# Kernel optimization log

Measured on AMD Instinct MI355X. Metric: run time of the kernel, lower is better.

## Reference

```python
import jax, jax.numpy as jnp
from jax import lax
import numpy as np

# Config (matches init_kwargs)
V = 8           # num_variables
E = 256         # embed_dim
LAGS = 4
W = 64          # window_size
STEP = 16       # step_size
K = 512         # num_tokens (codebook size)
B = 32
S = 8256        # samples; (S - W) % STEP == 0 -> T = 512 windows
T = (S - W) // STEP
CONV_OUT = (W - LAGS) // LAGS + 1   # 16 positions after strided conv


def setup_inputs() -> dict:
    key = jax.random.key(0)
    ks = jax.random.split(key, 6)
    x = jax.random.normal(ks[0], (B, V, S), dtype=jnp.float32)
    conv_w = jax.random.normal(ks[1], (E, V, LAGS), dtype=jnp.float32) * 0.1
    conv_b = jax.random.normal(ks[2], (E,), dtype=jnp.float32) * 0.01
    lin_w = jax.random.normal(ks[3], (E, E * CONV_OUT), dtype=jnp.float32) * 0.02
    lin_b = jax.random.normal(ks[4], (E,), dtype=jnp.float32) * 0.01
    codebook = jax.random.normal(ks[5], (K, E), dtype=jnp.float32)
    return {"x": x, "conv_w": conv_w, "conv_b": conv_b,
            "lin_w": lin_w, "lin_b": lin_b, "codebook": codebook}


def _encode_windows(x, conv_w, conv_b, lin_w, lin_b):
    # Extract all sliding windows at once: starts [T], offsets [W] -> idx [T, W]
    starts = jnp.arange(T) * STEP
    idx = starts[:, None] + jnp.arange(W)[None, :]
    xw = x[:, :, idx]                         # [B, V, T, W]
    xw = xw.transpose(0, 2, 1, 3).reshape(B * T, V, W)  # batch all windows
    # TCN encoder: strided Conv1d(V->E, kernel=LAGS, stride=LAGS) + ReLU
    y = lax.conv_general_dilated(
        xw, conv_w, window_strides=(LAGS,), padding='VALID',
        dimension_numbers=('NCH', 'OIH', 'NCH'))   # [B*T, E, CONV_OUT]
    y = jax.nn.relu(y + conv_b[None, :, None])
    # Flatten + Linear -> embedding per window
    e = y.reshape(B * T, E * CONV_OUT) @ lin_w.T + lin_b  # [B*T, E]
    return e


def reference(x, conv_w, conv_b, lin_w, lin_b, codebook):
    e = _encode_windows(x, conv_w, conv_b, lin_w, lin_b)   # [B*T, E]
    # Vector quantization: nearest codebook entry by L2 distance
    d = (jnp.sum(e * e, axis=1, keepdims=True)
         - 2.0 * (e @ codebook.T)
         + jnp.sum(codebook * codebook, axis=1)[None, :])  # [B*T, K]
    idx = jnp.argmin(d, axis=1)                            # [B*T]
    q = codebook[idx]                                      # [B*T, E]
    # straight-through estimator (standard VQ forward value == q)
    out = e + lax.stop_gradient(q - e)
    return out.reshape(B, T, E)
```

## Files before the change

kernel.cpp:

```cpp
#include <hip/hip_runtime.h>

typedef _Float16 f16;
typedef _Float16 f16x4 __attribute__((ext_vector_type(4)));
typedef _Float16 f16x8 __attribute__((ext_vector_type(8)));
typedef float    f32x16 __attribute__((ext_vector_type(16)));

#define NB 32
#define TTOT 512
#define SSN 8256
#define PT 2064
#define EE 256
#define KCB 512

#define YB   ((size_t)NB*EE*PT*2)
#define LWB  ((size_t)EE*4096*2)
#define CBB  ((size_t)KCB*EE*2)
#define EBB  ((size_t)16384*EE*2)
#define OFF_Y0  ((size_t)0)
#define OFF_Y1  (YB)
#define OFF_LW0 (2*YB)
#define OFF_LW1 (2*YB + LWB)
#define OFF_CB0 (2*YB + 2*LWB)
#define OFF_CB1 (2*YB + 2*LWB + CBB)
#define OFF_HN  (2*YB + 2*LWB + 2*CBB)
#define OFF_E0  (OFF_HN + 4096)
#define OFF_E1  (OFF_E0 + EBB)
#define WS_NEED (OFF_E1 + EBB)

#define INV2048 4.8828125e-4f

struct h2 { f16 hi, lo; };
__device__ __forceinline__ h2 split2(float v) {
  h2 r;
  r.hi = (f16)v;
  r.lo = (f16)((v - (float)r.hi) * 2048.0f);
  return r;
}

__device__ __forceinline__ f16x8 ldsfrag(const f16* p) {
  union { f16x8 v8; f16x4 v4[2]; } u;
  u.v4[0] = *(const f16x4*)p;
  u.v4[1] = *(const f16x4*)(p + 4);
  return u.v8;
}

#define MFMA16(a,b,c) __builtin_amdgcn_mfma_f32_32x32x16_f16(a, b, c, 0, 0, 0)

__global__ __launch_bounds__(256, 2)
void k01(const float* __restrict__ lin_w, const float* __restrict__ cbk,
         f16* __restrict__ lwp0, f16* __restrict__ lwp1,
         f16* __restrict__ cbp0, f16* __restrict__ cbp1, float* __restrict__ hn,
         const float* __restrict__ x, const float* __restrict__ cw,
         const float* __restrict__ cb, f16* __restrict__ y0, f16* __restrict__ y1)
{
  __shared__ float part[4][32];
  const int tid = threadIdx.x;
  const int bix = blockIdx.x;
  if (bix < 272) {
    const int bid = bix;
    if (bid < 256) {
      const int eo = bid, nb = eo >> 5, lo = eo & 31;
      const int ep = tid;
      const float* src = lin_w + (size_t)eo * 4096 + ep * 16;
      float f[16];
      *(float4*)(f + 0)  = ((const float4*)src)[0];
      *(float4*)(f + 4)  = ((const float4*)src)[1];
      *(float4*)(f + 8)  = ((const float4*)src)[2];
      *(float4*)(f + 12) = ((const float4*)src)[3];
      union { f16x8 v; f16 e[8]; } a0, a1, b0, b1;
#pragma unroll
      for (int i = 0; i < 8; ++i) {
        { h2 s = split2(f[i]);     a0.e[i] = s.hi; a1.e[i] = s.lo; }
        { h2 s = split2(f[i + 8]); b0.e[i] = s.hi; b1.e[i] = s.lo; }
      }
      const size_t base = ((size_t)nb * 16384 + (size_t)ep * 64 + lo) * 8;
      *(f16x8*)(lwp0 + base)       = a0.v;
      *(f16x8*)(lwp0 + base + 256) = b0.v;
      *(f16x8*)(lwp1 + base)       = a1.v;
      *(f16x8*)(lwp1 + base + 256) = b1.v;
    } else {
      const int jb = bid - 256;
      const int lane = tid & 63, ksg = tid >> 6;
      const int hi = lane >> 5, lo = lane & 31;
      const int j = jb * 32 + lo;
      float s = 0.f;
#pragma unroll
      for (int kq = 0; kq < 4; ++kq) {
        const int ks = ksg * 4 + kq;
        const float* src = cbk + (size_t)j * 256 + ks * 16 + 8 * hi;
        float f[8];
        *(float4*)(f + 0) = ((const float4*)src)[0];
        *(float4*)(f + 4) = ((const float4*)src)[1];
        union { f16x8 v; f16 e[8]; } h0, h1;
#pragma unroll
        for (int i = 0; i < 8; ++i) {
          s = fmaf(f[i], f[i], s);
          h2 t = split2(f[i]); h0.e[i] = t.hi; h1.e[i] = t.lo;
        }
        const size_t base = ((size_t)jb * 1024 + (size_t)ks * 64 + lane) * 8;
        *(f16x8*)(cbp0 + base) = h0.v;
        *(f16x8*)(cbp1 + base) = h1.v;
      }
      s += __shfl_xor(s, 32, 64);
      if (lane < 32) part[ksg][lane] = s;
      __syncthreads();
      if (tid < 32)
        hn[jb * 32 + tid] = 0.5f * (part[0][tid] + part[1][tid] + part[2][tid] + part[3][tid]);
    }
  } else {
    const int bid = bix - 272;
    const int b = bid / 18, rem = bid % 18;
    const int eq = rem / 9, ptile = rem % 9;
    const int p = ptile * 256 + tid;
    const bool valid = p < PT;
    const int pc = valid ? p : (PT - 1);
    float4 xv[8];
#pragma unroll
    for (int v = 0; v < 8; ++v)
      xv[v] = *(const float4*)(x + ((size_t)b * 8 + v) * SSN + 4 * pc);
    const int e0 = eq * 128;
    float4 wc[8], wn[8];
#pragma unroll
    for (int v = 0; v < 8; ++v) wc[v] = *(const float4*)(cw + (size_t)e0 * 32 + v * 4);
    for (int ep = e0; ep < e0 + 128; ++ep) {
      const int epn = (ep + 1 < e0 + 128) ? ep + 1 : ep;
#pragma unroll
      for (int v = 0; v < 8; ++v) wn[v] = *(const float4*)(cw + (size_t)epn * 32 + v * 4);
      float a = cb[ep];
#pragma unroll
      for (int v = 0; v < 8; ++v) {
        a = fmaf(xv[v].x, wc[v].x, a);
        a = fmaf(xv[v].y, wc[v].y, a);
        a = fmaf(xv[v].z, wc[v].z, a);
        a = fmaf(xv[v].w, wc[v].w, a);
      }
      a = fmaxf(a, 0.f);
      if (valid) {
        const h2 s = split2(a);
        const size_t o = ((size_t)b * EE + ep) * PT + p;
        y0[o] = s.hi; y1[o] = s.lo;
      }
#pragma unroll
      for (int v = 0; v < 8; ++v) wc[v] = wn[v];
    }
  }
}

__global__ __launch_bounds__(512, 1)
void k2_linear(const f16* __restrict__ yh0, const f16* __restrict__ yh1,
               const f16* __restrict__ lwp0, const f16* __restrict__ lwp1,
               const float* __restrict__ lin_b,
               f16* __restrict__ eh0, f16* __restrict__ eh1)
{
  __shared__ __align__(16) f16 ysh[2][2][4][528];
  __shared__ __align__(16) f16 bsh[2][4][4][2][512];
  const int tid = threadIdx.x;
  const int sw = (blockIdx.x & 7) * 32 + (blockIdx.x >> 3);
  const int nh = sw >> 7, mt = sw & 127;
  const int b = mt >> 2;
  const int p0 = (mt & 3) * 512;
  const int lane = tid & 63, wv = tid >> 6;
  const int m = wv >> 1, nq = wv & 1;
  const int hi = lane >> 5, lo = lane & 31;
  const int aoff = 4 * (m * 32 + lo) + 8 * hi;

  const int bke = wv >> 1;
  const int bnb0 = (wv & 1) * 2;
  const f16* bs[2][2];
#pragma unroll
  for (int j = 0; j < 2; ++j) {
    bs[j][0] = lwp0 + ((size_t)(nh * 4 + bnb0 + j) * 256) * 512 + lane * 8;
    bs[j][1] = lwp1 + ((size_t)(nh * 4 + bnb0 + j) * 256) * 512 + lane * 8;
  }
  const int ylimb = wv >> 2, yke = wv & 3;
  const f16* ysrcp = ylimb ? yh1 : yh0;
  const size_t ybase0 = ((size_t)b * EE + yke) * PT + p0 + lane * 8;

  f32x16 accH[2], accL[2];
#pragma unroll
  for (int n = 0; n < 2; ++n)
#pragma unroll
    for (int r = 0; r < 16; ++r) { accH[n][r] = 0.f; accL[n][r] = 0.f; }

  {
    const size_t epo = (size_t)bke * 512;
    float4 br[4];
#pragma unroll
    for (int i = 0; i < 4; ++i) br[i] = *(const float4*)(bs[i >> 1][i & 1] + epo);
    const float4 ya = *(const float4*)(ysrcp + ybase0);
    float4 yb{};
    if (lane < 2) yb = *(const float4*)(ysrcp + ybase0 + 512);
#pragma unroll
    for (int i = 0; i < 4; ++i)
      *(float4*)&bsh[0][bke][bnb0 + (i >> 1)][i & 1][lane * 8] = br[i];
    f16* yd = &ysh[0][ylimb][yke][lane * 8];
    *(float4*)yd = ya;
    if (lane < 2) *(float4*)(yd + 512) = yb;
  }
  __syncthreads();

  for (int ss = 0; ss < 64; ++ss) {
    const int cur = ss & 1;
    const int ssn = (ss < 63) ? ss + 1 : 63;
    const size_t epo = (size_t)(ssn * 4 + bke) * 512;
    float4 br[4];
#pragma unroll
    for (int i = 0; i < 4; ++i) br[i] = *(const float4*)(bs[i >> 1][i & 1] + epo);
    const size_t yb0 = ybase0 + (size_t)ssn * 4 * PT;
    const float4 ya = *(const float4*)(ysrcp + yb0);
    float4 yb{};
    if (lane < 2) yb = *(const float4*)(ysrcp + yb0 + 512);

#pragma unroll
    for (int ke = 0; ke < 4; ++ke) {
      const f16x8 a0 = ldsfrag(&ysh[cur][0][ke][aoff]);
      const f16x8 a1 = ldsfrag(&ysh[cur][1][ke][aoff]);
#pragma unroll
      for (int n = 0; n < 2; ++n) {
        const f16x8 b0 = *(const f16x8*)&bsh[cur][ke][nq * 2 + n][0][lane * 8];
        const f16x8 b1 = *(const f16x8*)&bsh[cur][ke][nq * 2 + n][1][lane * 8];
        accH[n] = MFMA16(a0, b0, accH[n]);
        accL[n] = MFMA16(a0, b1, accL[n]);
        accL[n] = MFMA16(a1, b0, accL[n]);
      }
    }
    {
      const int nxt = cur ^ 1;
#pragma unroll
      for (int i = 0; i < 4; ++i)
        *(float4*)&bsh[nxt][bke][bnb0 + (i >> 1)][i & 1][lane * 8] = br[i];
      f16* yd = &ysh[nxt][ylimb][yke][lane * 8];
      *(float4*)yd = ya;
      if (lane < 2) *(float4*)(yd + 512) = yb;
    }
    __syncthreads();
  }

#pragma unroll
  for (int n = 0; n < 2; ++n) {
    const int eo = nh * 128 + (nq * 2 + n) * 32 + lo;
    const float lb = lin_b[eo];
#pragma unroll
    for (int r = 0; r < 16; ++r) {
      const int wloc = m * 32 + (r & 3) + 8 * (r >> 2) + 4 * hi;
      const float v = accH[n][r] + accL[n][r] * INV2048 + lb;
      const h2 s = split2(v);
      const size_t o = (size_t)(mt * 128 + wloc) * EE + eo;
      eh0[o] = s.hi; eh1[o] = s.lo;
    }
  }
}

__global__ __launch_bounds__(512, 1)
void k3_dist(const f16* __restrict__ eh0, const f16* __restrict__ eh1,
             const f16* __restrict__ cbp0, const f16* __restrict__ cbp1,
             const float* __restrict__ hn, const float* __restrict__ cbk,
             float* __restrict__ out)
{
  __shared__ __align__(16) f16 esh[2][64][136];
  __shared__ float scs[4][64];
  __shared__ int   scj[4][64];
  __shared__ int   bestj[64];
  const int tid = threadIdx.x;
  const int w0 = blockIdx.x * 64;
  const int lane = tid & 63, wv = tid >> 6;
  const int m = wv & 1, jg = wv >> 1;
  const int hi = lane >> 5, lo = lane & 31;

  const f16* pBp[4][2];
  float hnv[4];
#pragma unroll
  for (int q = 0; q < 4; ++q) {
    const int jb = jg * 4 + q;
    pBp[q][0] = cbp0 + ((size_t)jb * 1024 + lane) * 8;
    pBp[q][1] = cbp1 + ((size_t)jb * 1024 + lane) * 8;
    hnv[q] = hn[jb * 32 + lo];
  }
  f32x16 accH[4], accL[4];
#pragma unroll
  for (int q = 0; q < 4; ++q)
#pragma unroll
    for (int r = 0; r < 16; ++r) { accH[q][r] = 0.f; accL[q][r] = 0.f; }

  const int ar = m * 32 + lo;
  f16x8 BA[4][2], BB[4][2];
#pragma unroll
  for (int q = 0; q < 4; ++q) {
    BA[q][0] = *(const f16x8*)(pBp[q][0]);
    BA[q][1] = *(const f16x8*)(pBp[q][1]);
  }

  for (int kh = 0; kh < 2; ++kh) {
    if (kh) __syncthreads();
    {
      const int r = tid >> 3, c8 = tid & 7;
      const f16* s0 = eh0 + (size_t)(w0 + r) * EE + kh * 128;
      const f16* s1 = eh1 + (size_t)(w0 + r) * EE + kh * 128;
#pragma unroll
      for (int i = 0; i < 2; ++i) {
        const int c = (c8 * 2 + i) * 8;
        *(float4*)&esh[0][r][c] = *(const float4*)(s0 + c);
        *(float4*)&esh[1][r][c] = *(const float4*)(s1 + c);
      }
    }
    __syncthreads();
#pragma unroll
    for (int ksl = 0; ksl < 8; ++ksl) {
      const int ks = kh * 8 + ksl;
      const int ksn = (ks < 15) ? ks + 1 : 15;
      const f16x8 a0 = *(const f16x8*)(&esh[0][ar][0] + ksl * 16 + 8 * hi);
      const f16x8 a1 = *(const f16x8*)(&esh[1][ar][0] + ksl * 16 + 8 * hi);
      if ((ks & 1) == 0) {
#pragma unroll
        for (int q = 0; q < 4; ++q) {
          BB[q][0] = *(const f16x8*)(pBp[q][0] + (size_t)ksn * 512);
          BB[q][1] = *(const f16x8*)(pBp[q][1] + (size_t)ksn * 512);
        }
#pragma unroll
        for (int q = 0; q < 4; ++q) {
          accH[q] = MFMA16(a0, BA[q][0], accH[q]);
          accL[q] = MFMA16(a0, BA[q][1], accL[q]);
          accL[q] = MFMA16(a1, BA[q][0], accL[q]);
        }
      } else {
#pragma unroll
        for (int q = 0; q < 4; ++q) {
          BA[q][0] = *(const f16x8*)(pBp[q][0] + (size_t)ksn * 512);
          BA[q][1] = *(const f16x8*)(pBp[q][1] + (size_t)ksn * 512);
        }
#pragma unroll
        for (int q = 0; q < 4; ++q) {
          accH[q] = MFMA16(a0, BB[q][0], accH[q]);
          accL[q] = MFMA16(a0, BB[q][1], accL[q]);
          accL[q] = MFMA16(a1, BB[q][0], accL[q]);
        }
      }
    }
  }

#pragma unroll
  for (int r = 0; r < 16; ++r) {
    float bs = accH[0][r] + accL[0][r] * INV2048 - hnv[0];
    int   bj = (jg * 4 + 0) * 32 + lo;
#pragma unroll
    for (int q = 1; q < 4; ++q) {
      const float s = accH[q][r] + accL[q][r] * INV2048 - hnv[q];
      const int   j = (jg * 4 + q) * 32 + lo;
      if (s > bs) { bs = s; bj = j; }
    }
#pragma unroll
    for (int d = 1; d < 32; d <<= 1) {
      const float os = __shfl_xor(bs, d, 64);
      const int   oj = __shfl_xor(bj, d, 64);
      if (os > bs || (os == bs && oj < bj)) { bs = os; bj = oj; }
    }
    if (lo == 0) {
      const int wloc = m * 32 + (r & 3) + 8 * (r >> 2) + 4 * hi;
      scs[jg][wloc] = bs; scj[jg][wloc] = bj;
    }
  }
  __syncthreads();
  if (tid < 64) {
    float bs = scs[0][tid]; int bj = scj[0][tid];
#pragma unroll
    for (int g = 1; g < 4; ++g) {
      const float s = scs[g][tid]; const int j = scj[g][tid];
      if (s > bs || (s == bs && j < bj)) { bs = s; bj = j; }
    }
    bestj[tid] = bj;
  }
  __syncthreads();
  {
    const int rr = tid >> 6;
    const int c4 = (tid & 63) * 4;
#pragma unroll
    for (int pass = 0; pass < 8; ++pass) {
      const int r = pass * 8 + rr;
      const int jb = bestj[r];
      const float4 v = *(const float4*)(cbk + (size_t)jb * EE + c4);
      *(float4*)(out + (size_t)(w0 + r) * EE + c4) = v;
    }
  }
}

#define V 8
#define LAGS 4
#define WIN 64
#define STEP 16
#define CONV_OUT 16
#define WPB 16
#define TPB 256
#define NWORD 19
#define YSTRIDE 80
#define XSPAN 304
#define FOFF_YS   0
#define FOFF_XS   10240
#define FOFF_ES   10240
#define FOFF_SC   0
#define FOFF_SI   4096
#define FOFF_PS   8192
#define FOFF_PI   8448
#define FOFF_IW   8704
#define SMEM_FLOATS 14336

__device__ __forceinline__ float f4get(const float4& v, int i) {
  return i == 0 ? v.x : (i == 1 ? v.y : (i == 2 ? v.z : v.w));
}

__device__ __forceinline__ float conv_one(const float* xs, int p, const float4* cw, float cb0) {
  float a = cb0;
#pragma unroll
  for (int v = 0; v < V; ++v) {
    const float4 xv = *(const float4*)(xs + v * XSPAN + 4 * p);
    a = fmaf(xv.x, cw[v].x, a);
    a = fmaf(xv.y, cw[v].y, a);
    a = fmaf(xv.z, cw[v].z, a);
    a = fmaf(xv.w, cw[v].w, a);
  }
  return fmaxf(a, 0.0f);
}

__global__ __launch_bounds__(TPB, 2)
void tok_fused(const float* __restrict__ x, const float* __restrict__ conv_w,
               const float* __restrict__ conv_b, const float* __restrict__ lin_w,
               const float* __restrict__ lin_b, const float* __restrict__ cbk,
               float* __restrict__ out)
{
  __shared__ float smem[SMEM_FLOATS];
  float* ys = smem + FOFF_YS;
  float* xs = smem + FOFF_XS;
  float* es = smem + FOFF_ES;
  float* sc = smem + FOFF_SC;
  int*   si = (int*)(smem + FOFF_SI);
  float* ps = smem + FOFF_PS;
  int*   pi = (int*)(smem + FOFF_PI);
  int*   iw = (int*)(smem + FOFF_IW);
  const int tid = threadIdx.x;
  const int b   = blockIdx.x >> 5;
  const int t0  = (blockIdx.x & 31) * WPB;
  const float* xb = x + (size_t)b * V * SSN + (size_t)t0 * STEP;
#pragma unroll
  for (int v = 0; v < V; ++v)
    for (int j = tid; j < XSPAN; j += TPB)
      xs[v * XSPAN + j] = xb[(size_t)v * SSN + j];
  double accd[WPB];
#pragma unroll
  for (int w = 0; w < WPB; ++w) accd[w] = 0.0;
  for (int half = 0; half < 2; ++half) {
    __syncthreads();
    {
      const int ep  = half * 128 + (tid >> 1);
      const int row = ep & 127;
      float4 cw[V];
      const float4* cwp = (const float4*)(conv_w + (size_t)ep * (V * LAGS));
#pragma unroll
      for (int v = 0; v < V; ++v) cw[v] = cwp[v];
      const float cb0 = conv_b[ep];
      const int c0 = (tid & 1) ? 10 : 0;
      const int c1 = (tid & 1) ? NWORD : 10;
      for (int c = c0; c < c1; ++c) {
        const int p = 4 * c;
        float r0 = conv_one(xs, p + 0, cw, cb0);
        float r1 = conv_one(xs, p + 1, cw, cb0);
        float r2 = conv_one(xs, p + 2, cw, cb0);
        float r3 = conv_one(xs, p + 3, cw, cb0);
        *(float4*)(ys + row * YSTRIDE + 4 * c) = make_float4(r0, r1, r2, r3);
      }
    }
    __syncthreads();
    const float* lwbase = lin_w + (size_t)tid * (EE * CONV_OUT) + half * (128 * CONV_OUT);
    float4 nA, nB, nC, nD;
    {
      const float4* p4 = (const float4*)(lwbase);
      nA = p4[0]; nB = p4[1]; nC = p4[2]; nD = p4[3];
    }
    for (int er = 0; er < 128; ++er) {
      const float4 lA = nA, lB = nB, lC = nC, lD = nD;
      const int ern = (er + 1) & 127;
      {
        const float4* p4 = (const float4*)(lwbase + ern * CONV_OUT);
        nA = p4[0]; nB = p4[1]; nC = p4[2]; nD = p4[3];
      }
      float4 yr[NWORD];
      const float4* yp = (const float4*)(ys + er * YSTRIDE);
#pragma unroll
      for (int q = 0; q < NWORD; ++q) yr[q] = yp[q];
      float it[WPB];
#pragma unroll
      for (int w = 0; w < WPB; ++w) it[w] = 0.0f;
#pragma unroll
      for (int o = 0; o < CONV_OUT; ++o) {
        const float lw_o = f4get(o < 4 ? lA : (o < 8 ? lB : (o < 12 ? lC : lD)), o & 3);
#pragma unroll
        for (int w = 0; w < WPB; ++w) {
          const int p = 4 * w + o;
          it[w] = fmaf(lw_o, f4get(yr[p >> 2], p & 3), it[w]);
        }
      }
#pragma unroll
      for (int w = 0; w < WPB; ++w) accd[w] += (double)it[w];
    }
  }
#pragma unroll
  for (int w = 0; w < WPB; ++w)
    es[w * EE + tid] = (float)accd[w] + lin_b[tid];
  __syncthreads();
  float s_best[WPB];
  int   i_best[WPB];
#pragma unroll
  for (int jj = 0; jj < 2; ++jj) {
    const int j = tid + jj * 256;
    const float4* cbp = (const float4*)(cbk + (size_t)j * EE);
    double sdd[WPB];
    float  sd32[WPB];
#pragma unroll
    for (int w = 0; w < WPB; ++w) { sdd[w] = 0.0; sd32[w] = 0.f; }
    double ndd = 0.0;
    float  nd32 = 0.f;
    float4 c4n = cbp[0];
    for (int i16 = 0; i16 < 4; ++i16) {
      for (int i4i = 0; i4i < 16; ++i4i) {
        const int i4 = i16 * 16 + i4i;
        const float4 c4 = c4n;
        c4n = cbp[(i4 + 1 <= 63) ? (i4 + 1) : 63];
        nd32 = fmaf(c4.x, c4.x, nd32);
        nd32 = fmaf(c4.y, c4.y, nd32);
        nd32 = fmaf(c4.z, c4.z, nd32);
        nd32 = fmaf(c4.w, c4.w, nd32);
#pragma unroll
        for (int w = 0; w < WPB; ++w) {
          const float4 e4 = *(const float4*)(es + w * EE + i4 * 4);
          sd32[w] = fmaf(c4.x, e4.x, sd32[w]);
          sd32[w] = fmaf(c4.y, e4.y, sd32[w]);
          sd32[w] = fmaf(c4.z, e4.z, sd32[w]);
          sd32[w] = fmaf(c4.w, e4.w, sd32[w]);
        }
      }
#pragma unroll
      for (int w = 0; w < WPB; ++w) { sdd[w] += (double)sd32[w]; sd32[w] = 0.f; }
      ndd += (double)nd32; nd32 = 0.f;
    }
#pragma unroll
    for (int w = 0; w < WPB; ++w) {
      const float s = (float)(sdd[w] - 0.5 * ndd);
      if (jj == 0) { s_best[w] = s; i_best[w] = j; }
      else if (s > s_best[w]) { s_best[w] = s; i_best[w] = j; }
    }
  }
#pragma unroll
  for (int w = 0; w < WPB; ++w) {
    sc[w * EE + tid] = s_best[w];
    si[w * EE + tid] = i_best[w];
  }
  __syncthreads();
  {
    const int w = tid >> 4, seg = tid & 15;
    float mm = -INFINITY; int mi = 0x7fffffff;
    for (int t = seg * 16; t < seg * 16 + 16; ++t) {
      const float s = sc[w * EE + t];
      const int   jx = si[w * EE + t];
      if (s > mm || (s == mm && jx < mi)) { mm = s; mi = jx; }
    }
    ps[w * 16 + seg] = mm; pi[w * 16 + seg] = mi;
  }
  __syncthreads();
  if (tid < WPB) {
    const int w = tid;
    float mm = -INFINITY; int mi = 0x7fffffff;
    for (int t = 0; t < 16; ++t) {
      const float s = ps[w * 16 + t];
      const int   jx = pi[w * 16 + t];
      if (s > mm || (s == mm && jx < mi)) { mm = s; mi = jx; }
    }
    iw[w] = mi;
  }
  __syncthreads();
  const size_t outb = ((size_t)b * TTOT + t0) * EE;
#pragma unroll
  for (int w = 0; w < WPB; ++w)
    out[outb + (size_t)w * EE + tid] = cbk[(size_t)iw[w] * EE + tid];
}

extern "C" void kernel_launch(void* const* d_in, const int* in_sizes, int n_in,
                              void* d_out, int out_size, void* d_ws, size_t ws_size,
                              hipStream_t stream) {
  const float* x      = (const float*)d_in[0];
  const float* conv_w = (const float*)d_in[1];
  const float* conv_b = (const float*)d_in[2];
  const float* lin_w  = (const float*)d_in[3];
  const float* lin_b  = (const float*)d_in[4];
  const float* cbk    = (const float*)d_in[5];
  float* out = (float*)d_out;

  if (ws_size < WS_NEED) {
    tok_fused<<<dim3(32 * 32), dim3(TPB), 0, stream>>>(x, conv_w, conv_b, lin_w, lin_b, cbk, out);
    return;
  }
  char* ws = (char*)d_ws;
  f16*   y0   = (f16*)(ws + OFF_Y0);
  f16*   y1   = (f16*)(ws + OFF_Y1);
  f16*   lwp0 = (f16*)(ws + OFF_LW0);
  f16*   lwp1 = (f16*)(ws + OFF_LW1);
  f16*   cbp0 = (f16*)(ws + OFF_CB0);
  f16*   cbp1 = (f16*)(ws + OFF_CB1);
  float* hn   = (float*)(ws + OFF_HN);
  f16*   e0   = (f16*)(ws + OFF_E0);
  f16*   e1   = (f16*)(ws + OFF_E1);

  k01<<<848, 256, 0, stream>>>(lin_w, cbk, lwp0, lwp1, cbp0, cbp1, hn,
                               x, conv_w, conv_b, y0, y1);
  k2_linear<<<256, 512, 0, stream>>>(y0, y1, lwp0, lwp1, lin_b, e0, e1);
  k3_dist <<<256, 512, 0, stream>>>(e0, e1, cbp0, cbp1, hn, cbk, out);
}
```

Baseline: 185.3 us.

## Give each wave a 2x2 MFMA tile in k2_linear with 256 threads

The linear GEMM kernel drops from 512 to 256 threads per block. Each wave now computes a 2x2 grid of 32x32 output tiles, so every A and B fragment read from LDS feeds two MFMAs, halving LDS reads per MFMA. Global loads are issued two tiles ahead, with registers holding the next tile while the current one is computed. This doubles accumulator register use per thread and leaves fewer waves per CU to hide latency.

Result: slower. 308.0 us (+66.2%).

```diff
diff --git a/kernel.cpp b/kernel.cpp
--- a/kernel.cpp
+++ b/kernel.cpp
@@ -146,7 +146,7 @@
   }
 }
 
-__global__ __launch_bounds__(512, 1)
+__global__ __launch_bounds__(256, 1)
 void k2_linear(const f16* __restrict__ yh0, const f16* __restrict__ yh1,
                const f16* __restrict__ lwp0, const f16* __restrict__ lwp1,
                const float* __restrict__ lin_b,
@@ -160,95 +160,118 @@
   const int b = mt >> 2;
   const int p0 = (mt & 3) * 512;
   const int lane = tid & 63, wv = tid >> 6;
-  const int m = wv >> 1, nq = wv & 1;
+  const int mg = wv >> 1, ng = wv & 1;
   const int hi = lane >> 5, lo = lane & 31;
-  const int aoff = 4 * (m * 32 + lo) + 8 * hi;
-
-  const int bke = wv >> 1;
-  const int bnb0 = (wv & 1) * 2;
-  const f16* bs[2][2];
+  int aoffs[2];
+#pragma unroll
+  for (int m2 = 0; m2 < 2; ++m2)
+    aoffs[m2] = 4 * ((mg * 2 + m2) * 32 + lo) + 8 * hi;
+
+  const f16* pBsrc[8];
+#pragma unroll
+  for (int i = 0; i < 8; ++i) {
+    const int nb = i >> 1, limb = i & 1;
+    const f16* base = limb ? lwp1 : lwp0;
+    pBsrc[i] = base + ((size_t)(nh * 4 + nb) * 256 + wv) * 512 + lane * 8;
+  }
+  const f16* pYsrc[2];
 #pragma unroll
   for (int j = 0; j < 2; ++j) {
-    bs[j][0] = lwp0 + ((size_t)(nh * 4 + bnb0 + j) * 256) * 512 + lane * 8;
-    bs[j][1] = lwp1 + ((size_t)(nh * 4 + bnb0 + j) * 256) * 512 + lane * 8;
-  }
-  const int ylimb = wv >> 2, yke = wv & 3;
-  const f16* ysrcp = ylimb ? yh1 : yh0;
-  const size_t ybase0 = ((size_t)b * EE + yke) * PT + p0 + lane * 8;
-
-  f32x16 accH[2], accL[2];
-#pragma unroll
-  for (int n = 0; n < 2; ++n)
-#pragma unroll
-    for (int r = 0; r < 16; ++r) { accH[n][r] = 0.f; accL[n][r] = 0.f; }
-
-  {
-    const size_t epo = (size_t)bke * 512;
-    float4 br[4];
-#pragma unroll
-    for (int i = 0; i < 4; ++i) br[i] = *(const float4*)(bs[i >> 1][i & 1] + epo);
-    const float4 ya = *(const float4*)(ysrcp + ybase0);
-    float4 yb{};
-    if (lane < 2) yb = *(const float4*)(ysrcp + ybase0 + 512);
-#pragma unroll
-    for (int i = 0; i < 4; ++i)
-      *(float4*)&bsh[0][bke][bnb0 + (i >> 1)][i & 1][lane * 8] = br[i];
-    f16* yd = &ysh[0][ylimb][yke][lane * 8];
-    *(float4*)yd = ya;
-    if (lane < 2) *(float4*)(yd + 512) = yb;
-  }
+    const int r = wv * 2 + j, limb = r >> 2, ke = r & 3;
+    const f16* base = limb ? yh1 : yh0;
+    pYsrc[j] = base + ((size_t)b * EE + ke) * PT + p0 + lane * 8;
+  }
+  const int yrow[2] = { wv * 2, wv * 2 + 1 };
+
+  f32x16 accH[2][2], accL[2][2];
+#pragma unroll
+  for (int m2 = 0; m2 < 2; ++m2)
+#pragma unroll
+    for (int n2 = 0; n2 < 2; ++n2)
+#pragma unroll
+      for (int r = 0; r < 16; ++r) { accH[m2][n2][r] = 0.f; accL[m2][n2][r] = 0.f; }
+
+  float4 br[8], yr[2], ye[2];
+  const bool yext = lane < 2;
+
+#define LOAD_TILE(tt) do {                                                     \
+    const size_t bo = (size_t)(tt) * 2048;                                     \
+    _Pragma("unroll")                                                          \
+    for (int i = 0; i < 8; ++i) br[i] = *(const float4*)(pBsrc[i] + bo);       \
+    const size_t yo = (size_t)(tt) * 4 * PT;                                   \
+    _Pragma("unroll")                                                          \
+    for (int j = 0; j < 2; ++j) {                                              \
+      yr[j] = *(const float4*)(pYsrc[j] + yo);                                 \
+      if (yext) ye[j] = *(const float4*)(pYsrc[j] + yo + 512);                 \
+    }                                                                          \
+  } while (0)
+
+#define WRITE_TILE(bb) do {                                                    \
+    _Pragma("unroll")                                                          \
+    for (int i = 0; i < 8; ++i)                                                \
+      *(float4*)&bsh[bb][wv][i >> 1][i & 1][lane * 8] = br[i];                 \
+    _Pragma("unroll")                                                          \
+    for (int j = 0; j < 2; ++j) {                                              \
+      const int r = yrow[j];                                                   \
+      f16* yd = &ysh[bb][r >> 2][r & 3][lane * 8];                             \
+      *(float4*)yd = yr[j];                                                    \
+      if (yext) *(float4*)(yd + 512) = ye[j];                                  \
+    }                                                                          \
+  } while (0)
+
+  LOAD_TILE(0);
+  WRITE_TILE(0);
+  LOAD_TILE(1);
   __syncthreads();
 
   for (int ss = 0; ss < 64; ++ss) {
     const int cur = ss & 1;
-    const int ssn = (ss < 63) ? ss + 1 : 63;
-    const size_t epo = (size_t)(ssn * 4 + bke) * 512;
-    float4 br[4];
-#pragma unroll
-    for (int i = 0; i < 4; ++i) br[i] = *(const float4*)(bs[i >> 1][i & 1] + epo);
-    const size_t yb0 = ybase0 + (size_t)ssn * 4 * PT;
-    const float4 ya = *(const float4*)(ysrcp + yb0);
-    float4 yb{};
-    if (lane < 2) yb = *(const float4*)(ysrcp + yb0 + 512);
+    WRITE_TILE(cur ^ 1);
+    const int tl = (ss + 2 < 64) ? ss + 2 : 63;
+    LOAD_TILE(tl);
 
 #pragma unroll
     for (int ke = 0; ke < 4; ++ke) {
-      const f16x8 a0 = ldsfrag(&ysh[cur][0][ke][aoff]);
-      const f16x8 a1 = ldsfrag(&ysh[cur][1][ke][aoff]);
-#pragma unroll
-      for (int n = 0; n < 2; ++n) {
-        const f16x8 b0 = *(const f16x8*)&bsh[cur][ke][nq * 2 + n][0][lane * 8];
-        const f16x8 b1 = *(const f16x8*)&bsh[cur][ke][nq * 2 + n][1][lane * 8];
-        accH[n] = MFMA16(a0, b0, accH[n]);
-        accL[n] = MFMA16(a0, b1, accL[n]);
-        accL[n] = MFMA16(a1, b0, accL[n]);
-      }
-    }
-    {
-      const int nxt = cur ^ 1;
-#pragma unroll
-      for (int i = 0; i < 4; ++i)
-        *(float4*)&bsh[nxt][bke][bnb0 + (i >> 1)][i & 1][lane * 8] = br[i];
-      f16* yd = &ysh[nxt][ylimb][yke][lane * 8];
-      *(float4*)yd = ya;
-      if (lane < 2) *(float4*)(yd + 512) = yb;
+      f16x8 a[2][2], bb[2][2];
+#pragma unroll
+      for (int m2 = 0; m2 < 2; ++m2) {
+        a[m2][0] = ldsfrag(&ysh[cur][0][ke][aoffs[m2]]);
+        a[m2][1] = ldsfrag(&ysh[cur][1][ke][aoffs[m2]]);
+      }
+#pragma unroll
+      for (int n2 = 0; n2 < 2; ++n2) {
+        bb[n2][0] = *(const f16x8*)&bsh[cur][ke][ng * 2 + n2][0][lane * 8];
+        bb[n2][1] = *(const f16x8*)&bsh[cur][ke][ng * 2 + n2][1][lane * 8];
+      }
+#pragma unroll
+      for (int m2 = 0; m2 < 2; ++m2)
+#pragma unroll
+        for (int n2 = 0; n2 < 2; ++n2) {
+          accH[m2][n2] = MFMA16(a[m2][0], bb[n2][0], accH[m2][n2]);
+          accL[m2][n2] = MFMA16(a[m2][0], bb[n2][1], accL[m2][n2]);
+          accL[m2][n2] = MFMA16(a[m2][1], bb[n2][0], accL[m2][n2]);
+        }
     }
     __syncthreads();
   }
 
 #pragma unroll
-  for (int n = 0; n < 2; ++n) {
-    const int eo = nh * 128 + (nq * 2 + n) * 32 + lo;
-    const float lb = lin_b[eo];
-#pragma unroll
-    for (int r = 0; r < 16; ++r) {
-      const int wloc = m * 32 + (r & 3) + 8 * (r >> 2) + 4 * hi;
-      const float v = accH[n][r] + accL[n][r] * INV2048 + lb;
-      const h2 s = split2(v);
-      const size_t o = (size_t)(mt * 128 + wloc) * EE + eo;
-      eh0[o] = s.hi; eh1[o] = s.lo;
-    }
-  }
+  for (int m2 = 0; m2 < 2; ++m2)
+#pragma unroll
+    for (int n2 = 0; n2 < 2; ++n2) {
+      const int eo = nh * 128 + (ng * 2 + n2) * 32 + lo;
+      const float lb = lin_b[eo];
+#pragma unroll
+      for (int r = 0; r < 16; ++r) {
+        const int wloc = (mg * 2 + m2) * 32 + (r & 3) + 8 * (r >> 2) + 4 * hi;
+        const float v = accH[m2][n2][r] + accL[m2][n2][r] * INV2048 + lb;
+        const h2 s = split2(v);
+        const size_t o = (size_t)(mt * 128 + wloc) * EE + eo;
+        eh0[o] = s.hi; eh1[o] = s.lo;
+      }
+    }
+#undef LOAD_TILE
+#undef WRITE_TILE
 }
 
 __global__ __launch_bounds__(512, 1)
@@ -609,6 +632,6 @@
 
   k01<<<848, 256, 0, stream>>>(lin_w, cbk, lwp0, lwp1, cbp0, cbp1, hn,
                                x, conv_w, conv_b, y0, y1);
-  k2_linear<<<256, 512, 0, stream>>>(y0, y1, lwp0, lwp1, lin_b, e0, e1);
+  k2_linear<<<256, 256, 0, stream>>>(y0, y1, lwp0, lwp1, lin_b, e0, e1);
   k3_dist <<<256, 512, 0, stream>>>(e0, e1, cbp0, cbp1, hn, cbk, out);
 }
```

## Split linear GEMM over K into two halves with atomic fp32 accumulation

Applied to the files above, without the earlier changes.

The linear layer kernel now splits the reduction dimension in two, launching twice as many blocks that each accumulate partial results into an fp32 buffer with atomicAdd. LDS double buffering is dropped to allow more resident blocks. Bias addition and the hi/lo fp16 split move into the distance kernel's load stage. This targets low occupancy on a 256-block launch, at the cost of a memset, fp32 atomics, extra global traffic and an extra barrier per step.

Result: slower. 272.4 us (+47.0%).

```diff
diff --git a/kernel.cpp b/kernel.cpp
--- a/kernel.cpp
+++ b/kernel.cpp
@@ -26,6 +26,7 @@
 #define OFF_E0  (OFF_HN + 4096)
 #define OFF_E1  (OFF_E0 + EBB)
 #define WS_NEED (OFF_E1 + EBB)
+#define PACC_BYTES ((size_t)16384*EE*4)
 
 #define INV2048 4.8828125e-4f
 
@@ -146,35 +147,31 @@
   }
 }
 
-__global__ __launch_bounds__(512, 1)
-void k2_linear(const f16* __restrict__ yh0, const f16* __restrict__ yh1,
-               const f16* __restrict__ lwp0, const f16* __restrict__ lwp1,
-               const float* __restrict__ lin_b,
-               f16* __restrict__ eh0, f16* __restrict__ eh1)
+__global__ __launch_bounds__(512, 4)
+void k2p(const f16* __restrict__ yh0, const f16* __restrict__ yh1,
+         const f16* __restrict__ lwp0, const f16* __restrict__ lwp1,
+         float* __restrict__ pacc)
 {
-  __shared__ __align__(16) f16 ysh[2][2][4][528];
-  __shared__ __align__(16) f16 bsh[2][4][4][2][512];
+  __shared__ __align__(16) f16 ysh[2][4][528];
+  __shared__ __align__(16) f16 bsh[4][4][2][512];
   const int tid = threadIdx.x;
-  const int sw = (blockIdx.x & 7) * 32 + (blockIdx.x >> 3);
-  const int nh = sw >> 7, mt = sw & 127;
-  const int b = mt >> 2;
+  const int sw = (blockIdx.x & 7) * 64 + (blockIdx.x >> 3);
+  const int kh = sw >> 8;
+  const int rest = sw & 255;
+  const int mt = rest >> 1, nh = rest & 1;
+  const int b  = mt >> 2;
   const int p0 = (mt & 3) * 512;
   const int lane = tid & 63, wv = tid >> 6;
-  const int m = wv >> 1, nq = wv & 1;
+  const int mg = wv >> 1, nqw = wv & 1;
   const int hi = lane >> 5, lo = lane & 31;
-  const int aoff = 4 * (m * 32 + lo) + 8 * hi;
-
-  const int bke = wv >> 1;
-  const int bnb0 = (wv & 1) * 2;
-  const f16* bs[2][2];
-#pragma unroll
-  for (int j = 0; j < 2; ++j) {
-    bs[j][0] = lwp0 + ((size_t)(nh * 4 + bnb0 + j) * 256) * 512 + lane * 8;
-    bs[j][1] = lwp1 + ((size_t)(nh * 4 + bnb0 + j) * 256) * 512 + lane * 8;
-  }
+
+  const int bke = wv >> 1, bnb0 = (wv & 1) * 2;
+  const f16* bs00 = lwp0 + ((size_t)(nh * 4 + bnb0) * 256 + kh * 128 + bke) * 512 + lane * 8;
+  const f16* bs01 = lwp1 + ((size_t)(nh * 4 + bnb0) * 256 + kh * 128 + bke) * 512 + lane * 8;
   const int ylimb = wv >> 2, yke = wv & 3;
   const f16* ysrcp = ylimb ? yh1 : yh0;
-  const size_t ybase0 = ((size_t)b * EE + yke) * PT + p0 + lane * 8;
+  const size_t ybase0 = ((size_t)b * EE + kh * 128 + yke) * PT + p0 + lane * 8;
+  const bool yext = lane < 2;
 
   f32x16 accH[2], accL[2];
 #pragma unroll
@@ -182,77 +179,71 @@
 #pragma unroll
     for (int r = 0; r < 16; ++r) { accH[n][r] = 0.f; accL[n][r] = 0.f; }
 
-  {
-    const size_t epo = (size_t)bke * 512;
-    float4 br[4];
-#pragma unroll
-    for (int i = 0; i < 4; ++i) br[i] = *(const float4*)(bs[i >> 1][i & 1] + epo);
-    const float4 ya = *(const float4*)(ysrcp + ybase0);
-    float4 yb{};
-    if (lane < 2) yb = *(const float4*)(ysrcp + ybase0 + 512);
-#pragma unroll
-    for (int i = 0; i < 4; ++i)
-      *(float4*)&bsh[0][bke][bnb0 + (i >> 1)][i & 1][lane * 8] = br[i];
-    f16* yd = &ysh[0][ylimb][yke][lane * 8];
-    *(float4*)yd = ya;
-    if (lane < 2) *(float4*)(yd + 512) = yb;
-  }
+  float4 br[4], ya; float4 yb{};
+
+#define K2LOAD(ss_) do {                                                       \
+    const size_t bo = (size_t)(ss_) * 2048;                                    \
+    br[0] = *(const float4*)(bs00 + bo);                                       \
+    br[1] = *(const float4*)(bs01 + bo);                                       \
+    br[2] = *(const float4*)(bs00 + 131072 + bo);                              \
+    br[3] = *(const float4*)(bs01 + 131072 + bo);                              \
+    const size_t yo = ybase0 + (size_t)(ss_) * (4 * PT);                       \
+    ya = *(const float4*)(ysrcp + yo);                                         \
+    if (yext) yb = *(const float4*)(ysrcp + yo + 512);                         \
+  } while (0)
+
+#define K2WRITE() do {                                                         \
+    *(float4*)&bsh[bke][bnb0    ][0][lane * 8] = br[0];                        \
+    *(float4*)&bsh[bke][bnb0    ][1][lane * 8] = br[1];                        \
+    *(float4*)&bsh[bke][bnb0 + 1][0][lane * 8] = br[2];                        \
+    *(float4*)&bsh[bke][bnb0 + 1][1][lane * 8] = br[3];                        \
+    f16* yd = &ysh[ylimb][yke][lane * 8];                                      \
+    *(float4*)yd = ya;                                                         \
+    if (yext) *(float4*)(yd + 512) = yb;                                       \
+  } while (0)
+
+  K2LOAD(0);
+  K2WRITE();
   __syncthreads();
 
-  for (int ss = 0; ss < 64; ++ss) {
-    const int cur = ss & 1;
-    const int ssn = (ss < 63) ? ss + 1 : 63;
-    const size_t epo = (size_t)(ssn * 4 + bke) * 512;
-    float4 br[4];
-#pragma unroll
-    for (int i = 0; i < 4; ++i) br[i] = *(const float4*)(bs[i >> 1][i & 1] + epo);
-    const size_t yb0 = ybase0 + (size_t)ssn * 4 * PT;
-    const float4 ya = *(const float4*)(ysrcp + yb0);
-    float4 yb{};
-    if (lane < 2) yb = *(const float4*)(ysrcp + yb0 + 512);
-
+  for (int ss = 0; ss < 32; ++ss) {
+    K2LOAD((ss < 31) ? ss + 1 : 31);
+
+    const int aoff = 4 * (mg * 32 + lo) + 8 * hi;
 #pragma unroll
     for (int ke = 0; ke < 4; ++ke) {
-      const f16x8 a0 = ldsfrag(&ysh[cur][0][ke][aoff]);
-      const f16x8 a1 = ldsfrag(&ysh[cur][1][ke][aoff]);
+      const f16x8 a0 = ldsfrag(&ysh[0][ke][aoff]);
+      const f16x8 a1 = ldsfrag(&ysh[1][ke][aoff]);
 #pragma unroll
       for (int n = 0; n < 2; ++n) {
-        const f16x8 b0 = *(const f16x8*)&bsh[cur][ke][nq * 2 + n][0][lane * 8];
-        const f16x8 b1 = *(const f16x8*)&bsh[cur][ke][nq * 2 + n][1][lane * 8];
+        const f16x8 b0 = *(const f16x8*)&bsh[ke][nqw * 2 + n][0][lane * 8];
+        const f16x8 b1 = *(const f16x8*)&bsh[ke][nqw * 2 + n][1][lane * 8];
         accH[n] = MFMA16(a0, b0, accH[n]);
         accL[n] = MFMA16(a0, b1, accL[n]);
         accL[n] = MFMA16(a1, b0, accL[n]);
       }
     }
-    {
-      const int nxt = cur ^ 1;
-#pragma unroll
-      for (int i = 0; i < 4; ++i)
-        *(float4*)&bsh[nxt][bke][bnb0 + (i >> 1)][i & 1][lane * 8] = br[i];
-      f16* yd = &ysh[nxt][ylimb][yke][lane * 8];
-      *(float4*)yd = ya;
-      if (lane < 2) *(float4*)(yd + 512) = yb;
-    }
     __syncthreads();
-  }
+    K2WRITE();
+    __syncthreads();
+  }
+#undef K2LOAD
+#undef K2WRITE
 
 #pragma unroll
   for (int n = 0; n < 2; ++n) {
-    const int eo = nh * 128 + (nq * 2 + n) * 32 + lo;
-    const float lb = lin_b[eo];
+    const int eo = nh * 128 + (nqw * 2 + n) * 32 + lo;
 #pragma unroll
     for (int r = 0; r < 16; ++r) {
-      const int wloc = m * 32 + (r & 3) + 8 * (r >> 2) + 4 * hi;
-      const float v = accH[n][r] + accL[n][r] * INV2048 + lb;
-      const h2 s = split2(v);
-      const size_t o = (size_t)(mt * 128 + wloc) * EE + eo;
-      eh0[o] = s.hi; eh1[o] = s.lo;
+      const int wloc = mg * 32 + (r & 3) + 8 * (r >> 2) + 4 * hi;
+      const float v = accH[n][r] + accL[n][r] * INV2048;
+      atomicAdd(&pacc[(size_t)(mt * 128 + wloc) * EE + eo], v);
     }
   }
 }
 
 __global__ __launch_bounds__(512, 1)
-void k3_dist(const f16* __restrict__ eh0, const f16* __restrict__ eh1,
+void k3_dist(const float* __restrict__ pacc, const float* __restrict__ lin_b,
              const f16* __restrict__ cbp0, const f16* __restrict__ cbp1,
              const float* __restrict__ hn, const float* __restrict__ cbk,
              float* __restrict__ out)
@@ -294,14 +285,25 @@
     if (kh) __syncthreads();
     {
       const int r = tid >> 3, c8 = tid & 7;
-      const f16* s0 = eh0 + (size_t)(w0 + r) * EE + kh * 128;
-      const f16* s1 = eh1 + (size_t)(w0 + r) * EE + kh * 128;
-#pragma unroll
-      for (int i = 0; i < 2; ++i) {
-        const int c = (c8 * 2 + i) * 8;
-        *(float4*)&esh[0][r][c] = *(const float4*)(s0 + c);
-        *(float4*)&esh[1][r][c] = *(const float4*)(s1 + c);
-      }
+      const float* ps = pacc + (size_t)(w0 + r) * EE + kh * 128 + c8 * 16;
+      const float* bsp = lin_b + kh * 128 + c8 * 16;
+      float f[16], bb[16];
+#pragma unroll
+      for (int i = 0; i < 4; ++i) {
+        *(float4*)(f + 4 * i)  = ((const float4*)ps)[i];
+        *(float4*)(bb + 4 * i) = ((const float4*)bsp)[i];
+      }
+      union { f16x8 v; f16 e[8]; } h0[2], h1[2];
+#pragma unroll
+      for (int i = 0; i < 16; ++i) {
+        const h2 s = split2(f[i] + bb[i]);
+        h0[i >> 3].e[i & 7] = s.hi;
+        h1[i >> 3].e[i & 7] = s.lo;
+      }
+      *(f16x8*)&esh[0][r][c8 * 16]     = h0[0].v;
+      *(f16x8*)&esh[0][r][c8 * 16 + 8] = h0[1].v;
+      *(f16x8*)&esh[1][r][c8 * 16]     = h1[0].v;
+      *(f16x8*)&esh[1][r][c8 * 16 + 8] = h1[1].v;
     }
     __syncthreads();
 #pragma unroll
@@ -604,11 +606,11 @@
   f16*   cbp0 = (f16*)(ws + OFF_CB0);
   f16*   cbp1 = (f16*)(ws + OFF_CB1);
   float* hn   = (float*)(ws + OFF_HN);
-  f16*   e0   = (f16*)(ws + OFF_E0);
-  f16*   e1   = (f16*)(ws + OFF_E1);
-
+  float* pacc = (float*)(ws + OFF_E0);
+
+  hipMemsetAsync(pacc, 0, PACC_BYTES, stream);
   k01<<<848, 256, 0, stream>>>(lin_w, cbk, lwp0, lwp1, cbp0, cbp1, hn,
                                x, conv_w, conv_b, y0, y1);
-  k2_linear<<<256, 512, 0, stream>>>(y0, y1, lwp0, lwp1, lin_b, e0, e1);
-  k3_dist <<<256, 512, 0, stream>>>(e0, e1, cbp0, cbp1, hn, cbk, out);
-}
+  k2p<<<512, 512, 0, stream>>>(y0, y1, lwp0, lwp1, pacc);
+  k3_dist<<<256, 512, 0, stream>>>(pacc, lin_b, cbp0, cbp1, hn, cbk, out);
+}
```

## Split linear GEMM along K into two partial-sum halves, reduce in distance kernel

Applied to the files above, without the earlier changes.

The linear layer GEMM is split into two K halves, giving 512 blocks instead of 256 and more parallelism across CUs. Each half writes fp32 partial sums to a new workspace region. The distance kernel adds the halves plus bias and splits the result into hi/lo fp16 before the codebook MFMA. This costs extra fp32 traffic for the partial buffers and needs a larger workspace, with a fallback to the old path when the workspace is too small.

New measurement: 252.6 us. 36.3% more time.

```diff
diff --git a/kernel.cpp b/kernel.cpp
--- a/kernel.cpp
+++ b/kernel.cpp
@@ -26,6 +26,9 @@
 #define OFF_E0  (OFF_HN + 4096)
 #define OFF_E1  (OFF_E0 + EBB)
 #define WS_NEED (OFF_E1 + EBB)
+#define PACC_BYTES ((size_t)16384*EE*4)
+#define OFF_P1  (WS_NEED)
+#define WS_NEED2 (WS_NEED + PACC_BYTES)
 
 #define INV2048 4.8828125e-4f
 
@@ -146,6 +149,252 @@
   }
 }
 
+__global__ __launch_bounds__(512, 4)
+void k2p(const f16* __restrict__ yh0, const f16* __restrict__ yh1,
+         const f16* __restrict__ lwp0, const f16* __restrict__ lwp1,
+         float* __restrict__ pacc0, float* __restrict__ pacc1)
+{
+  __shared__ __align__(16) f16 ysh[2][4][528];
+  __shared__ __align__(16) f16 bsh[4][4][2][512];
+  const int tid = threadIdx.x;
+  const int sw = (blockIdx.x & 7) * 64 + (blockIdx.x >> 3);
+  const int kh = sw >> 8;
+  const int rest = sw & 255;
+  const int mt = rest >> 1, nh = rest & 1;
+  const int b  = mt >> 2;
+  const int p0 = (mt & 3) * 512;
+  const int lane = tid & 63, wv = tid >> 6;
+  const int mg = wv >> 1, nqw = wv & 1;
+  const int hi = lane >> 5, lo = lane & 31;
+
+  const int bke = wv >> 1, bnb0 = (wv & 1) * 2;
+  const f16* bs00 = lwp0 + ((size_t)(nh * 4 + bnb0) * 256 + kh * 128 + bke) * 512 + lane * 8;
+  const f16* bs01 = lwp1 + ((size_t)(nh * 4 + bnb0) * 256 + kh * 128 + bke) * 512 + lane * 8;
+  const int ylimb = wv >> 2, yke = wv & 3;
+  const f16* ysrcp = ylimb ? yh1 : yh0;
+  const size_t ybase0 = ((size_t)b * EE + kh * 128 + yke) * PT + p0 + lane * 8;
+  const bool yext = lane < 2;
+
+  f32x16 accH[2], accL[2];
+#pragma unroll
+  for (int n = 0; n < 2; ++n)
+#pragma unroll
+    for (int r = 0; r < 16; ++r) { accH[n][r] = 0.f; accL[n][r] = 0.f; }
+
+  float4 br[4], ya; float4 yb{};
+
+#define K2LOAD(ss_) do {                                                       \
+    const size_t bo = (size_t)(ss_) * 2048;                                    \
+    br[0] = *(const float4*)(bs00 + bo);                                       \
+    br[1] = *(const float4*)(bs01 + bo);                                       \
+    br[2] = *(const float4*)(bs00 + 131072 + bo);                              \
+    br[3] = *(const float4*)(bs01 + 131072 + bo);                              \
+    const size_t yo = ybase0 + (size_t)(ss_) * (4 * PT);                       \
+    ya = *(const float4*)(ysrcp + yo);                                         \
+    if (yext) yb = *(const float4*)(ysrcp + yo + 512);                         \
+  } while (0)
+
+#define K2WRITE() do {                                                         \
+    *(float4*)&bsh[bke][bnb0    ][0][lane * 8] = br[0];                        \
+    *(float4*)&bsh[bke][bnb0    ][1][lane * 8] = br[1];                        \
+    *(float4*)&bsh[bke][bnb0 + 1][0][lane * 8] = br[2];                        \
+    *(float4*)&bsh[bke][bnb0 + 1][1][lane * 8] = br[3];                        \
+    f16* yd = &ysh[ylimb][yke][lane * 8];                                      \
+    *(float4*)yd = ya;                                                         \
+    if (yext) *(float4*)(yd + 512) = yb;                                       \
+  } while (0)
+
+  K2LOAD(0);
+  K2WRITE();
+  __syncthreads();
+
+  for (int ss = 0; ss < 32; ++ss) {
+    K2LOAD((ss < 31) ? ss + 1 : 31);
+
+    const int aoff = 4 * (mg * 32 + lo) + 8 * hi;
+#pragma unroll
+    for (int ke = 0; ke < 4; ++ke) {
+      const f16x8 a0 = ldsfrag(&ysh[0][ke][aoff]);
+      const f16x8 a1 = ldsfrag(&ysh[1][ke][aoff]);
+#pragma unroll
+      for (int n = 0; n < 2; ++n) {
+        const f16x8 b0 = *(const f16x8*)&bsh[ke][nqw * 2 + n][0][lane * 8];
+        const f16x8 b1 = *(const f16x8*)&bsh[ke][nqw * 2 + n][1][lane * 8];
+        accH[n] = MFMA16(a0, b0, accH[n]);
+        accL[n] = MFMA16(a0, b1, accL[n]);
+        accL[n] = MFMA16(a1, b0, accL[n]);
+      }
+    }
+    __syncthreads();
+    K2WRITE();
+    __syncthreads();
+  }
+#undef K2LOAD
+#undef K2WRITE
+
+  float* pacc = kh ? pacc1 : pacc0;
+#pragma unroll
+  for (int n = 0; n < 2; ++n) {
+    const int eo = nh * 128 + (nqw * 2 + n) * 32 + lo;
+#pragma unroll
+    for (int r = 0; r < 16; ++r) {
+      const int wloc = mg * 32 + (r & 3) + 8 * (r >> 2) + 4 * hi;
+      pacc[(size_t)(mt * 128 + wloc) * EE + eo] = accH[n][r] + accL[n][r] * INV2048;
+    }
+  }
+}
+
+__global__ __launch_bounds__(512, 1)
+void k3s(const float* __restrict__ pacc0, const float* __restrict__ pacc1,
+         const float* __restrict__ lin_b,
+         const f16* __restrict__ cbp0, const f16* __restrict__ cbp1,
+         const float* __restrict__ hn, const float* __restrict__ cbk,
+         float* __restrict__ out)
+{
+  __shared__ __align__(16) f16 esh[2][64][136];
+  __shared__ float scs[4][64];
+  __shared__ int   scj[4][64];
+  __shared__ int   bestj[64];
+  const int tid = threadIdx.x;
+  const int w0 = blockIdx.x * 64;
+  const int lane = tid & 63, wv = tid >> 6;
+  const int m = wv & 1, jg = wv >> 1;
+  const int hi = lane >> 5, lo = lane & 31;
+
+  const f16* pBp[4][2];
+  float hnv[4];
+#pragma unroll
+  for (int q = 0; q < 4; ++q) {
+    const int jb = jg * 4 + q;
+    pBp[q][0] = cbp0 + ((size_t)jb * 1024 + lane) * 8;
+    pBp[q][1] = cbp1 + ((size_t)jb * 1024 + lane) * 8;
+    hnv[q] = hn[jb * 32 + lo];
+  }
+  f32x16 accH[4], accL[4];
+#pragma unroll
+  for (int q = 0; q < 4; ++q)
+#pragma unroll
+    for (int r = 0; r < 16; ++r) { accH[q][r] = 0.f; accL[q][r] = 0.f; }
+
+  const int ar = m * 32 + lo;
+  f16x8 BA[4][2], BB[4][2];
+#pragma unroll
+  for (int q = 0; q < 4; ++q) {
+    BA[q][0] = *(const f16x8*)(pBp[q][0]);
+    BA[q][1] = *(const f16x8*)(pBp[q][1]);
+  }
+
+  for (int kh = 0; kh < 2; ++kh) {
+    if (kh) __syncthreads();
+    {
+      const int r = tid >> 3, c8 = tid & 7;
+      const size_t idx = (size_t)(w0 + r) * EE + kh * 128 + c8 * 16;
+      const float* ps0 = pacc0 + idx;
+      const float* ps1 = pacc1 + idx;
+      const float* bsp = lin_b + kh * 128 + c8 * 16;
+      float f[16];
+#pragma unroll
+      for (int i = 0; i < 4; ++i) {
+        const float4 v0 = ((const float4*)ps0)[i];
+        const float4 v1 = ((const float4*)ps1)[i];
+        const float4 bb = ((const float4*)bsp)[i];
+        f[4 * i + 0] = v0.x + v1.x + bb.x;
+        f[4 * i + 1] = v0.y + v1.y + bb.y;
+        f[4 * i + 2] = v0.z + v1.z + bb.z;
+        f[4 * i + 3] = v0.w + v1.w + bb.w;
+      }
+      union { f16x8 v; f16 e[8]; } h0[2], h1[2];
+#pragma unroll
+      for (int i = 0; i < 16; ++i) {
+        const h2 s = split2(f[i]);
+        h0[i >> 3].e[i & 7] = s.hi;
+        h1[i >> 3].e[i & 7] = s.lo;
+      }
+      *(f16x8*)&esh[0][r][c8 * 16]     = h0[0].v;
+      *(f16x8*)&esh[0][r][c8 * 16 + 8] = h0[1].v;
+      *(f16x8*)&esh[1][r][c8 * 16]     = h1[0].v;
+      *(f16x8*)&esh[1][r][c8 * 16 + 8] = h1[1].v;
+    }
+    __syncthreads();
+#pragma unroll
+    for (int ksl = 0; ksl < 8; ++ksl) {
+      const int ks = kh * 8 + ksl;
+      const int ksn = (ks < 15) ? ks + 1 : 15;
+      const f16x8 a0 = *(const f16x8*)(&esh[0][ar][0] + ksl * 16 + 8 * hi);
+      const f16x8 a1 = *(const f16x8*)(&esh[1][ar][0] + ksl * 16 + 8 * hi);
+      if ((ks & 1) == 0) {
+#pragma unroll
+        for (int q = 0; q < 4; ++q) {
+          BB[q][0] = *(const f16x8*)(pBp[q][0] + (size_t)ksn * 512);
+          BB[q][1] = *(const f16x8*)(pBp[q][1] + (size_t)ksn * 512);
+        }
+#pragma unroll
+        for (int q = 0; q < 4; ++q) {
+          accH[q] = MFMA16(a0, BA[q][0], accH[q]);
+          accL[q] = MFMA16(a0, BA[q][1], accL[q]);
+          accL[q] = MFMA16(a1, BA[q][0], accL[q]);
+        }
+      } else {
+#pragma unroll
+        for (int q = 0; q < 4; ++q) {
+          BA[q][0] = *(const f16x8*)(pBp[q][0] + (size_t)ksn * 512);
+          BA[q][1] = *(const f16x8*)(pBp[q][1] + (size_t)ksn * 512);
+        }
+#pragma unroll
+        for (int q = 0; q < 4; ++q) {
+          accH[q] = MFMA16(a0, BB[q][0], accH[q]);
+          accL[q] = MFMA16(a0, BB[q][1], accL[q]);
+          accL[q] = MFMA16(a1, BB[q][0], accL[q]);
+        }
+      }
+    }
+  }
+
+#pragma unroll
+  for (int r = 0; r < 16; ++r) {
+    float bs = accH[0][r] + accL[0][r] * INV2048 - hnv[0];
+    int   bj = (jg * 4 + 0) * 32 + lo;
+#pragma unroll
+    for (int q = 1; q < 4; ++q) {
+      const float s = accH[q][r] + accL[q][r] * INV2048 - hnv[q];
+      const int   j = (jg * 4 + q) * 32 + lo;
+      if (s > bs) { bs = s; bj = j; }
+    }
+#pragma unroll
+    for (int d = 1; d < 32; d <<= 1) {
+      const float os = __shfl_xor(bs, d, 64);
+      const int   oj = __shfl_xor(bj, d, 64);
+      if (os > bs || (os == bs && oj < bj)) { bs = os; bj = oj; }
+    }
+    if (lo == 0) {
+      const int wloc = m * 32 + (r & 3) + 8 * (r >> 2) + 4 * hi;
+      scs[jg][wloc] = bs; scj[jg][wloc] = bj;
+    }
+  }
+  __syncthreads();
+  if (tid < 64) {
+    float bs = scs[0][tid]; int bj = scj[0][tid];
+#pragma unroll
+    for (int g = 1; g < 4; ++g) {
+      const float s = scs[g][tid]; const int j = scj[g][tid];
+      if (s > bs || (s == bs && j < bj)) { bs = s; bj = j; }
+    }
+    bestj[tid] = bj;
+  }
+  __syncthreads();
+  {
+    const int rr = tid >> 6;
+    const int c4 = (tid & 63) * 4;
+#pragma unroll
+    for (int pass = 0; pass < 8; ++pass) {
+      const int r = pass * 8 + rr;
+      const int jb = bestj[r];
+      const float4 v = *(const float4*)(cbk + (size_t)jb * EE + c4);
+      *(float4*)(out + (size_t)(w0 + r) * EE + c4) = v;
+    }
+  }
+}
+
 __global__ __launch_bounds__(512, 1)
 void k2_linear(const f16* __restrict__ yh0, const f16* __restrict__ yh1,
                const f16* __restrict__ lwp0, const f16* __restrict__ lwp1,
@@ -252,10 +501,10 @@
 }
 
 __global__ __launch_bounds__(512, 1)
-void k3_dist(const f16* __restrict__ eh0, const f16* __restrict__ eh1,
-             const f16* __restrict__ cbp0, const f16* __restrict__ cbp1,
-             const float* __restrict__ hn, const float* __restrict__ cbk,
-             float* __restrict__ out)
+void k3_old(const f16* __restrict__ eh0, const f16* __restrict__ eh1,
+            const f16* __restrict__ cbp0, const f16* __restrict__ cbp1,
+            const float* __restrict__ hn, const float* __restrict__ cbk,
+            float* __restrict__ out)
 {
   __shared__ __align__(16) f16 esh[2][64][136];
   __shared__ float scs[4][64];
@@ -604,11 +853,19 @@
   f16*   cbp0 = (f16*)(ws + OFF_CB0);
   f16*   cbp1 = (f16*)(ws + OFF_CB1);
   float* hn   = (float*)(ws + OFF_HN);
-  f16*   e0   = (f16*)(ws + OFF_E0);
-  f16*   e1   = (f16*)(ws + OFF_E1);
 
   k01<<<848, 256, 0, stream>>>(lin_w, cbk, lwp0, lwp1, cbp0, cbp1, hn,
                                x, conv_w, conv_b, y0, y1);
-  k2_linear<<<256, 512, 0, stream>>>(y0, y1, lwp0, lwp1, lin_b, e0, e1);
-  k3_dist <<<256, 512, 0, stream>>>(e0, e1, cbp0, cbp1, hn, cbk, out);
-}
+
+  if (ws_size >= WS_NEED2) {
+    float* pacc0 = (float*)(ws + OFF_E0);
+    float* pacc1 = (float*)(ws + OFF_P1);
+    k2p<<<512, 512, 0, stream>>>(y0, y1, lwp0, lwp1, pacc0, pacc1);
+    k3s<<<256, 512, 0, stream>>>(pacc0, pacc1, lin_b, cbp0, cbp1, hn, cbk, out);
+  } else {
+    f16* e0 = (f16*)(ws + OFF_E0);
+    f16* e1 = (f16*)(ws + OFF_E1);
+    k2_linear<<<256, 512, 0, stream>>>(y0, y1, lwp0, lwp1, lin_b, e0, e1);
+    k3_old<<<256, 512, 0, stream>>>(e0, e1, cbp0, cbp1, hn, cbk, out);
+  }
+}
```
